# Optimization experiments

Hardware: AMD Instinct MI355X
Metric: run time of the kernel (lower is better)

The kernel has to match this reference:

```python
import jax, jax.numpy as jnp
import numpy as np

NEG_SLOPE = 0.01  # torch F.leaky_relu_ default


def setup_inputs() -> dict:
    key = jax.random.key(0)
    k1, k2, k3, k4, k5 = jax.random.split(key, 5)
    N, Fin, Fout = 8192, 256, 128
    X = jax.random.normal(k1, (N, Fin), dtype=jnp.float32)
    adj = jax.random.randint(k2, (N, N), 0, 2, dtype=jnp.int32)
    W = jax.random.normal(k3, (Fout, Fin), dtype=jnp.float32) * 0.05
    b = jax.random.normal(k4, (Fout,), dtype=jnp.float32) * 0.05
    S = jax.random.normal(k5, (2 * Fout,), dtype=jnp.float32)
    return {"X": X, "adj": adj, "W": W, "b": b, "S": S}


def reference(X, adj, W, b, S):
    # X' = W X + b  -> (N, Fout)
    Xp = X @ W.T + b
    N, Fout = Xp.shape
    S_src, S_dst = S[:Fout], S[Fout:]
    # e_ij = leaky_relu(S . [x'_i ; x'_j]) = leaky_relu(S_src.x'_i + S_dst.x'_j)
    e = jax.nn.leaky_relu(
        (Xp @ S_src)[:, None] + (Xp @ S_dst)[None, :], NEG_SLOPE
    )  # (N, N)
    # neighbor set = nonzero entries of adj row plus self-loop
    mask = (adj != 0) | jnp.eye(N, dtype=bool)
    e = jnp.where(mask, e, -jnp.inf)
    attn = jax.nn.softmax(e, axis=1)  # segment softmax over each row's neighbors
    out = jax.nn.sigmoid(attn @ Xp)  # (N, Fout)
    return out
```

## Files before the change

kernel.cpp:

```cpp
#include <hip/hip_runtime.h>

typedef unsigned short u16;
typedef __attribute__((ext_vector_type(8))) u16 u16x8;
typedef __attribute__((ext_vector_type(8))) __bf16 bf16x8;
typedef __attribute__((ext_vector_type(4))) float f32x4;

#define NN 8192
#define FIN 256
#define FOUT 128

__device__ __forceinline__ u16 f2bf(float f) {
  unsigned u = __float_as_uint(f);
  u += 0x7fffu + ((u >> 16) & 1u);
  return (u16)(u >> 16);
}
__device__ __forceinline__ float bf2f(u16 s) {
  return __uint_as_float(((unsigned)s) << 16);
}

__global__ __launch_bounds__(256) void k_splitw(const float* __restrict__ W,
                                                u16* __restrict__ Whi,
                                                u16* __restrict__ Wlo) {
  int t = blockIdx.x * 256 + threadIdx.x;
  float w = W[t];
  u16 hi = f2bf(w);
  Whi[t] = hi;
  Wlo[t] = f2bf(w - bf2f(hi));
}

__global__ __launch_bounds__(256) void k_xp(const float* __restrict__ X,
    const u16* __restrict__ Whi, const u16* __restrict__ Wlo,
    const float* __restrict__ bias, const float* __restrict__ S,
    u16* __restrict__ Bsw, float* __restrict__ alphaA, float* __restrict__ cexpA,
    float* __restrict__ jbF, u16* __restrict__ jebA, u16* __restrict__ jeb2A) {
  __shared__ float Xs[32 * 129];
  __shared__ float Ss[256];
  const int tid = threadIdx.x;
  Ss[tid] = S[tid];
  const int i0 = blockIdx.x * 32;
  const int w = tid >> 6, l = tid & 63;
  const int mt = w & 1, nh = w >> 1;
  const int li = l & 15, quad = l >> 4;
  const int row = i0 + mt * 16 + li;

  f32x4 acc[4];
#pragma unroll
  for (int nt4 = 0; nt4 < 4; ++nt4) acc[nt4] = f32x4{0.f, 0.f, 0.f, 0.f};

  const float* xrow = X + (size_t)row * FIN + quad * 8;
  for (int k0 = 0; k0 < FIN; k0 += 32) {
    float4 xa = *(const float4*)(xrow + k0);
    float4 xb = *(const float4*)(xrow + k0 + 4);
    float xv[8] = {xa.x, xa.y, xa.z, xa.w, xb.x, xb.y, xb.z, xb.w};
    u16x8 ahiu, alou;
#pragma unroll
    for (int jj = 0; jj < 8; ++jj) {
      u16 h = f2bf(xv[jj]);
      ahiu[jj] = h;
      alou[jj] = f2bf(xv[jj] - bf2f(h));
    }
    bf16x8 ahi = __builtin_bit_cast(bf16x8, ahiu);
    bf16x8 alo = __builtin_bit_cast(bf16x8, alou);
#pragma unroll
    for (int nt4 = 0; nt4 < 4; ++nt4) {
      int f = nh * 64 + nt4 * 16 + li;
      size_t wofs = (size_t)f * FIN + k0 + quad * 8;
      bf16x8 bhi = __builtin_bit_cast(bf16x8, *(const u16x8*)(Whi + wofs));
      bf16x8 blo = __builtin_bit_cast(bf16x8, *(const u16x8*)(Wlo + wofs));
      acc[nt4] = __builtin_amdgcn_mfma_f32_16x16x32_bf16(ahi, bhi, acc[nt4], 0, 0, 0);
      acc[nt4] = __builtin_amdgcn_mfma_f32_16x16x32_bf16(alo, bhi, acc[nt4], 0, 0, 0);
      acc[nt4] = __builtin_amdgcn_mfma_f32_16x16x32_bf16(ahi, blo, acc[nt4], 0, 0, 0);
    }
  }
#pragma unroll
  for (int nt4 = 0; nt4 < 4; ++nt4) {
    int f = nh * 64 + nt4 * 16 + li;
    float bv = bias[f];
#pragma unroll
    for (int r = 0; r < 4; ++r)
      Xs[(mt * 16 + quad * 4 + r) * 129 + f] = acc[nt4][r] + bv;
  }
  __syncthreads();

#pragma unroll
  for (int s = 0; s < 2; ++s) {
    int nt = w + s * 4;
    int f = nt * 16 + li;
    int jl = quad * 8;
    u16x8 ou;
#pragma unroll
    for (int jj = 0; jj < 8; ++jj) ou[jj] = f2bf(Xs[(jl + jj) * 129 + f]);
    *(u16x8*)(Bsw + (((size_t)(i0 >> 5)) * 8 + nt) * 512 + (size_t)l * 8) = ou;
  }

  const int r = tid >> 3, sub = tid & 7;
  float pa = 0.f, pb = 0.f;
#pragma unroll
  for (int m = 0; m < 16; ++m) {
    int f = sub + m * 8;
    float x = Xs[r * 129 + f];
    pa += x * Ss[f];
    pb += x * Ss[128 + f];
  }
  pa += __shfl_xor(pa, 1); pa += __shfl_xor(pa, 2); pa += __shfl_xor(pa, 4);
  pb += __shfl_xor(pb, 1); pb += __shfl_xor(pb, 2); pb += __shfl_xor(pb, 4);
  if (sub == 0) {
    int i = i0 + r;
    alphaA[i] = pa;
    cexpA[i] = expf(-0.99f * pa);
    jbF[i] = pb;
    jebA[i] = f2bf(expf(pb));
    jeb2A[i] = f2bf(expf(0.01f * pb));
  }
}

__global__ __launch_bounds__(512, 2) void k_gat(const int* __restrict__ adj,
    const u16* __restrict__ Bsw, const float* __restrict__ alphaA,
    const float* __restrict__ cexpA, const float* __restrict__ jbF,
    const u16* __restrict__ jebA, const u16* __restrict__ jeb2A,
    float* __restrict__ out) {
  __shared__ float sacc[32 * 132];
  __shared__ float sden[32];
  const int tid = threadIdx.x;
  for (int t = tid; t < 32 * 132; t += 512) sacc[t] = 0.f;
  if (tid < 32) sden[tid] = 0.f;
  __syncthreads();

  const int w = tid >> 6, l = tid & 63;
  const int li = l & 15, quad = l >> 4;
  const int i0 = blockIdx.x * 32;
  const int im0 = i0 + li, im1 = im0 + 16;
  const float nega0 = -alphaA[im0], nega1 = -alphaA[im1];
  const float c0 = cexpA[im0], c1 = cexpA[im1];
  const int* ar0 = adj + (size_t)im0 * NN;
  const int* ar1 = adj + (size_t)im1 * NN;

  f32x4 acc0[8], acc1[8];
#pragma unroll
  for (int nt = 0; nt < 8; ++nt) {
    acc0[nt] = f32x4{0.f, 0.f, 0.f, 0.f};
    acc1[nt] = f32x4{0.f, 0.f, 0.f, 0.f};
  }
  float den0 = 0.f, den1 = 0.f;

  const int jbeg = w * 1024, jend = jbeg + 1024;
  for (int j0 = jbeg; j0 < jend; j0 += 32) {
    const int jq = j0 + quad * 8;
    int4 a00 = *(const int4*)(ar0 + jq);
    int4 a01 = *(const int4*)(ar0 + jq + 4);
    int4 a10 = *(const int4*)(ar1 + jq);
    int4 a11 = *(const int4*)(ar1 + jq + 4);
    float4 b0 = *(const float4*)(jbF + jq);
    float4 b1 = *(const float4*)(jbF + jq + 4);
    u16x8 ebj = *(const u16x8*)(jebA + jq);
    u16x8 e2j = *(const u16x8*)(jeb2A + jq);
    int a0v[8] = {a00.x, a00.y, a00.z, a00.w, a01.x, a01.y, a01.z, a01.w};
    int a1v[8] = {a10.x, a10.y, a10.z, a10.w, a11.x, a11.y, a11.z, a11.w};
    float bv[8] = {b0.x, b0.y, b0.z, b0.w, b1.x, b1.y, b1.z, b1.w};
    u16x8 af0, af1;
#pragma unroll
    for (int jj = 0; jj < 8; ++jj) {
      float bf = bv[jj];
      float eb = bf2f(ebj[jj]);
      float e2 = bf2f(e2j[jj]);
      int jg = jq + jj;
      float w0 = (bf >= nega0) ? eb : c0 * e2;
      w0 = (a0v[jj] != 0 || jg == im0) ? w0 : 0.f;
      u16 q0 = f2bf(w0);
      af0[jj] = q0;
      den0 += bf2f(q0);
      float w1 = (bf >= nega1) ? eb : c1 * e2;
      w1 = (a1v[jj] != 0 || jg == im1) ? w1 : 0.f;
      u16 q1 = f2bf(w1);
      af1[jj] = q1;
      den1 += bf2f(q1);
    }
    bf16x8 A0 = __builtin_bit_cast(bf16x8, af0);
    bf16x8 A1 = __builtin_bit_cast(bf16x8, af1);
    const u16* bb = Bsw + ((size_t)(j0 >> 5) * 8) * 512 + (size_t)l * 8;
#pragma unroll
    for (int nt = 0; nt < 8; ++nt) {
      bf16x8 B = __builtin_bit_cast(bf16x8, *(const u16x8*)(bb + nt * 512));
      acc0[nt] = __builtin_amdgcn_mfma_f32_16x16x32_bf16(A0, B, acc0[nt], 0, 0, 0);
      acc1[nt] = __builtin_amdgcn_mfma_f32_16x16x32_bf16(A1, B, acc1[nt], 0, 0, 0);
    }
  }

  den0 += __shfl_xor(den0, 16); den0 += __shfl_xor(den0, 32);
  den1 += __shfl_xor(den1, 16); den1 += __shfl_xor(den1, 32);
  if (l < 16) { atomicAdd(&sden[li], den0); atomicAdd(&sden[16 + li], den1); }

#pragma unroll
  for (int nt = 0; nt < 8; ++nt) {
#pragma unroll
    for (int r = 0; r < 4; ++r) {
      atomicAdd(&sacc[(quad * 4 + r) * 132 + nt * 16 + li], acc0[nt][r]);
      atomicAdd(&sacc[(16 + quad * 4 + r) * 132 + nt * 16 + li], acc1[nt][r]);
    }
  }
  __syncthreads();

  const int orow = l & 31, fh = l >> 5;
  const int fbase = w * 16 + fh * 8;
  const float* p = &sacc[orow * 132 + fbase];
  float4 v0 = *(const float4*)p;
  float4 v1 = *(const float4*)(p + 4);
  float rd = 1.f / sden[orow];
  float o[8] = {v0.x, v0.y, v0.z, v0.w, v1.x, v1.y, v1.z, v1.w};
#pragma unroll
  for (int jj = 0; jj < 8; ++jj) {
    float v = o[jj] * rd;
    o[jj] = 1.f / (1.f + __expf(-v));
  }
  float* op = out + (size_t)(i0 + orow) * FOUT + fbase;
  *(float4*)op = make_float4(o[0], o[1], o[2], o[3]);
  *(float4*)(op + 4) = make_float4(o[4], o[5], o[6], o[7]);
}

extern "C" void kernel_launch(void* const* d_in, const int* in_sizes, int n_in,
                              void* d_out, int out_size, void* d_ws, size_t ws_size,
                              hipStream_t stream) {
  const float* X = (const float*)d_in[0];
  const int* adj = (const int*)d_in[1];
  const float* W = (const float*)d_in[2];
  const float* bias = (const float*)d_in[3];
  const float* S = (const float*)d_in[4];
  float* out = (float*)d_out;

  char* ws = (char*)d_ws;
  u16* Bsw     = (u16*)(ws);
  u16* Whi     = (u16*)(ws + 2097152);
  u16* Wlo     = (u16*)(ws + 2162688);
  float* alphaA = (float*)(ws + 2228224);
  float* cexpA  = (float*)(ws + 2260992);
  float* jbF    = (float*)(ws + 2293760);
  u16* jebA    = (u16*)(ws + 2326528);
  u16* jeb2A   = (u16*)(ws + 2342912);

  hipLaunchKernelGGL(k_splitw, dim3(128), dim3(256), 0, stream, W, Whi, Wlo);
  hipLaunchKernelGGL(k_xp, dim3(256), dim3(256), 0, stream, X, Whi, Wlo, bias, S,
                     Bsw, alphaA, cexpA, jbF, jebA, jeb2A);
  hipLaunchKernelGGL(k_gat, dim3(256), dim3(512), 0, stream, adj, Bsw, alphaA, cexpA,
                     jbF, jebA, jeb2A, out);
}
```

Before: 476.0 us.

## Restructure GAT kernels: max-based weights, MFMA denominator, diagonal precompute, prefetch

The attention weight uses max(exp(b_j), c_i*exp(0.01 b_j)), which equals the leaky-relu exponential, so the per-element comparison and the alpha/jb arrays are no longer needed. The self-loop is handled by a precomputed diagonal weight that seeds the accumulators, so the per-element index comparison goes away. The row-sum denominator is computed with an extra MFMA against a ones vector instead of scalar adds. Both kernels now use 16 rows per block with twice as many blocks, adj loads are software-prefetched one iteration ahead, and truncation replaces rounding for the bf16 pack. This trades the reuse of B tiles across two row groups for more parallelism and a lighter inner loop, with small numeric differences from the truncation.

```diff
diff --git a/kernel.cpp b/kernel.cpp
--- a/kernel.cpp
+++ b/kernel.cpp
@@ -13,6 +13,9 @@
   unsigned u = __float_as_uint(f);
   u += 0x7fffu + ((u >> 16) & 1u);
   return (u16)(u >> 16);
+}
+__device__ __forceinline__ u16 f2bft(float f) {
+  return (u16)(__float_as_uint(f) >> 16);
 }
 __device__ __forceinline__ float bf2f(u16 s) {
   return __uint_as_float(((unsigned)s) << 16);
@@ -31,26 +34,32 @@
 __global__ __launch_bounds__(256) void k_xp(const float* __restrict__ X,
     const u16* __restrict__ Whi, const u16* __restrict__ Wlo,
     const float* __restrict__ bias, const float* __restrict__ S,
-    u16* __restrict__ Bsw, float* __restrict__ alphaA, float* __restrict__ cexpA,
-    float* __restrict__ jbF, u16* __restrict__ jebA, u16* __restrict__ jeb2A) {
-  __shared__ float Xs[32 * 129];
+    const int* __restrict__ adj,
+    u16* __restrict__ Bsw, float* __restrict__ cexpA,
+    u16* __restrict__ jebA, u16* __restrict__ jeb2A, float* __restrict__ diagW) {
+  __shared__ float Xs[16 * 260];
+  __shared__ float Xp[16 * 132];
   __shared__ float Ss[256];
   const int tid = threadIdx.x;
+  const int i0 = blockIdx.x * 16;
   Ss[tid] = S[tid];
-  const int i0 = blockIdx.x * 32;
-  const int w = tid >> 6, l = tid & 63;
-  const int mt = w & 1, nh = w >> 1;
-  const int li = l & 15, quad = l >> 4;
-  const int row = i0 + mt * 16 + li;
-
-  f32x4 acc[4];
-#pragma unroll
-  for (int nt4 = 0; nt4 < 4; ++nt4) acc[nt4] = f32x4{0.f, 0.f, 0.f, 0.f};
-
-  const float* xrow = X + (size_t)row * FIN + quad * 8;
+  {
+    int r = tid >> 4, c = (tid & 15) * 16;
+    const float* src = X + (size_t)(i0 + r) * FIN + c;
+    float* dst = Xs + r * 260 + c;
+#pragma unroll
+    for (int k = 0; k < 16; k += 4) *(float4*)(dst + k) = *(const float4*)(src + k);
+  }
+  __syncthreads();
+
+  const int w = tid >> 6, l = tid & 63, li = l & 15, quad = l >> 4;
+  f32x4 acc[2];
+  acc[0] = f32x4{0.f, 0.f, 0.f, 0.f};
+  acc[1] = f32x4{0.f, 0.f, 0.f, 0.f};
   for (int k0 = 0; k0 < FIN; k0 += 32) {
-    float4 xa = *(const float4*)(xrow + k0);
-    float4 xb = *(const float4*)(xrow + k0 + 4);
+    const float* xp = Xs + li * 260 + k0 + quad * 8;
+    float4 xa = *(const float4*)xp;
+    float4 xb = *(const float4*)(xp + 4);
     float xv[8] = {xa.x, xa.y, xa.z, xa.w, xb.x, xb.y, xb.z, xb.w};
     u16x8 ahiu, alou;
 #pragma unroll
@@ -62,159 +71,179 @@
     bf16x8 ahi = __builtin_bit_cast(bf16x8, ahiu);
     bf16x8 alo = __builtin_bit_cast(bf16x8, alou);
 #pragma unroll
-    for (int nt4 = 0; nt4 < 4; ++nt4) {
-      int f = nh * 64 + nt4 * 16 + li;
+    for (int t2 = 0; t2 < 2; ++t2) {
+      int f = (w * 2 + t2) * 16 + li;
       size_t wofs = (size_t)f * FIN + k0 + quad * 8;
       bf16x8 bhi = __builtin_bit_cast(bf16x8, *(const u16x8*)(Whi + wofs));
       bf16x8 blo = __builtin_bit_cast(bf16x8, *(const u16x8*)(Wlo + wofs));
-      acc[nt4] = __builtin_amdgcn_mfma_f32_16x16x32_bf16(ahi, bhi, acc[nt4], 0, 0, 0);
-      acc[nt4] = __builtin_amdgcn_mfma_f32_16x16x32_bf16(alo, bhi, acc[nt4], 0, 0, 0);
-      acc[nt4] = __builtin_amdgcn_mfma_f32_16x16x32_bf16(ahi, blo, acc[nt4], 0, 0, 0);
-    }
-  }
-#pragma unroll
-  for (int nt4 = 0; nt4 < 4; ++nt4) {
-    int f = nh * 64 + nt4 * 16 + li;
+      acc[t2] = __builtin_amdgcn_mfma_f32_16x16x32_bf16(ahi, bhi, acc[t2], 0, 0, 0);
+      acc[t2] = __builtin_amdgcn_mfma_f32_16x16x32_bf16(alo, bhi, acc[t2], 0, 0, 0);
+      acc[t2] = __builtin_amdgcn_mfma_f32_16x16x32_bf16(ahi, blo, acc[t2], 0, 0, 0);
+    }
+  }
+#pragma unroll
+  for (int t2 = 0; t2 < 2; ++t2) {
+    int f = (w * 2 + t2) * 16 + li;
     float bv = bias[f];
 #pragma unroll
     for (int r = 0; r < 4; ++r)
-      Xs[(mt * 16 + quad * 4 + r) * 129 + f] = acc[nt4][r] + bv;
-  }
-  __syncthreads();
-
-#pragma unroll
-  for (int s = 0; s < 2; ++s) {
-    int nt = w + s * 4;
-    int f = nt * 16 + li;
-    int jl = quad * 8;
+      Xp[(quad * 4 + r) * 132 + f] = acc[t2][r] + bv;
+  }
+  __syncthreads();
+
+  {
+    int li2 = tid & 15, q2sub = (tid >> 4) & 1, nt = tid >> 5;
+    int f = nt * 16 + li2;
+    int rb = q2sub * 8;
+    int q2 = ((i0 & 16) >> 3) + q2sub;
     u16x8 ou;
 #pragma unroll
-    for (int jj = 0; jj < 8; ++jj) ou[jj] = f2bf(Xs[(jl + jj) * 129 + f]);
-    *(u16x8*)(Bsw + (((size_t)(i0 >> 5)) * 8 + nt) * 512 + (size_t)l * 8) = ou;
-  }
-
-  const int r = tid >> 3, sub = tid & 7;
-  float pa = 0.f, pb = 0.f;
-#pragma unroll
-  for (int m = 0; m < 16; ++m) {
-    int f = sub + m * 8;
-    float x = Xs[r * 129 + f];
-    pa += x * Ss[f];
-    pb += x * Ss[128 + f];
-  }
-  pa += __shfl_xor(pa, 1); pa += __shfl_xor(pa, 2); pa += __shfl_xor(pa, 4);
-  pb += __shfl_xor(pb, 1); pb += __shfl_xor(pb, 2); pb += __shfl_xor(pb, 4);
-  if (sub == 0) {
+    for (int jj = 0; jj < 8; ++jj) ou[jj] = f2bf(Xp[(rb + jj) * 132 + f]);
+    *(u16x8*)(Bsw + ((size_t)(i0 >> 5) * 8 + nt) * 512 + (size_t)(q2 * 16 + li2) * 8) = ou;
+  }
+
+  {
+    int r = tid >> 4, sub = tid & 15;
+    float pa = 0.f, pb = 0.f;
+#pragma unroll
+    for (int m = 0; m < 8; ++m) {
+      float x = Xp[r * 132 + sub + m * 16];
+      pa += x * Ss[sub + m * 16];
+      pb += x * Ss[128 + sub + m * 16];
+    }
+    pa += __shfl_xor(pa, 1); pa += __shfl_xor(pa, 2);
+    pa += __shfl_xor(pa, 4); pa += __shfl_xor(pa, 8);
+    pb += __shfl_xor(pb, 1); pb += __shfl_xor(pb, 2);
+    pb += __shfl_xor(pb, 4); pb += __shfl_xor(pb, 8);
+    if (sub == 0) {
+      int i = i0 + r;
+      float cc = expf(-0.99f * pa);
+      u16 ebq = f2bf(expf(pb));
+      u16 e2q = f2bf(expf(0.01f * pb));
+      cexpA[i] = cc;
+      jebA[i] = ebq;
+      jeb2A[i] = e2q;
+      float wii = fmaxf(bf2f(ebq), cc * bf2f(e2q));
+      float wq = bf2f(f2bft(wii));
+      int ad = adj[(size_t)i * NN + i];
+      diagW[i] = (ad != 0) ? 0.f : wq;
+    }
+  }
+}
+
+__global__ __launch_bounds__(512, 4) void k_gat(const int* __restrict__ adj,
+    const u16* __restrict__ Bsw, const float* __restrict__ cexpA,
+    const u16* __restrict__ jebA, const u16* __restrict__ jeb2A,
+    const float* __restrict__ diagW, float* __restrict__ out) {
+  __shared__ float sacc[16 * 132];
+  __shared__ float sden[16];
+  const int tid = threadIdx.x;
+  const int i0 = blockIdx.x * 16;
+
+  {
+    int r = tid >> 5, f = (tid & 31) * 4;
     int i = i0 + r;
-    alphaA[i] = pa;
-    cexpA[i] = expf(-0.99f * pa);
-    jbF[i] = pb;
-    jebA[i] = f2bf(expf(pb));
-    jeb2A[i] = f2bf(expf(0.01f * pb));
-  }
-}
-
-__global__ __launch_bounds__(512, 2) void k_gat(const int* __restrict__ adj,
-    const u16* __restrict__ Bsw, const float* __restrict__ alphaA,
-    const float* __restrict__ cexpA, const float* __restrict__ jbF,
-    const u16* __restrict__ jebA, const u16* __restrict__ jeb2A,
-    float* __restrict__ out) {
-  __shared__ float sacc[32 * 132];
-  __shared__ float sden[32];
-  const int tid = threadIdx.x;
-  for (int t = tid; t < 32 * 132; t += 512) sacc[t] = 0.f;
-  if (tid < 32) sden[tid] = 0.f;
-  __syncthreads();
-
-  const int w = tid >> 6, l = tid & 63;
-  const int li = l & 15, quad = l >> 4;
-  const int i0 = blockIdx.x * 32;
-  const int im0 = i0 + li, im1 = im0 + 16;
-  const float nega0 = -alphaA[im0], nega1 = -alphaA[im1];
-  const float c0 = cexpA[im0], c1 = cexpA[im1];
-  const int* ar0 = adj + (size_t)im0 * NN;
-  const int* ar1 = adj + (size_t)im1 * NN;
-
-  f32x4 acc0[8], acc1[8];
-#pragma unroll
-  for (int nt = 0; nt < 8; ++nt) {
-    acc0[nt] = f32x4{0.f, 0.f, 0.f, 0.f};
-    acc1[nt] = f32x4{0.f, 0.f, 0.f, 0.f};
-  }
-  float den0 = 0.f, den1 = 0.f;
+    float dw = diagW[i];
+    size_t slotbase = (size_t)(i0 >> 5) * 8;
+    int laneq = ((i & 31) >> 3) * 16;
+    int elem = i & 7;
+    float4 v;
+    float* vp = &v.x;
+#pragma unroll
+    for (int k = 0; k < 4; ++k) {
+      int ff = f + k;
+      u16 xb = Bsw[(slotbase + (ff >> 4)) * 512 + (size_t)(laneq + (ff & 15)) * 8 + elem];
+      vp[k] = dw * bf2f(xb);
+    }
+    *(float4*)&sacc[r * 132 + f] = v;
+    if (tid < 16) sden[tid] = diagW[i0 + tid];
+  }
+  __syncthreads();
+
+  const int w = tid >> 6, l = tid & 63, li = l & 15, quad = l >> 4;
+  const int im = i0 + li;
+  const float c = cexpA[im];
+  const int* ar = adj + (size_t)im * NN;
+
+  f32x4 acc[8];
+#pragma unroll
+  for (int nt = 0; nt < 8; ++nt) acc[nt] = f32x4{0.f, 0.f, 0.f, 0.f};
+  f32x4 accD = f32x4{0.f, 0.f, 0.f, 0.f};
+
+  u16x8 onesu;
+#pragma unroll
+  for (int jj = 0; jj < 8; ++jj) onesu[jj] = 0x3F80;
+  const bf16x8 ONES = __builtin_bit_cast(bf16x8, onesu);
 
   const int jbeg = w * 1024, jend = jbeg + 1024;
+  const int qofs = quad * 8;
+
+  int4 ca0, ca1;
+  u16x8 ceb, ce2;
+  {
+    const int jq = jbeg + qofs;
+    ca0 = *(const int4*)(ar + jq);
+    ca1 = *(const int4*)(ar + jq + 4);
+    ceb = *(const u16x8*)(jebA + jq);
+    ce2 = *(const u16x8*)(jeb2A + jq);
+  }
   for (int j0 = jbeg; j0 < jend; j0 += 32) {
-    const int jq = j0 + quad * 8;
-    int4 a00 = *(const int4*)(ar0 + jq);
-    int4 a01 = *(const int4*)(ar0 + jq + 4);
-    int4 a10 = *(const int4*)(ar1 + jq);
-    int4 a11 = *(const int4*)(ar1 + jq + 4);
-    float4 b0 = *(const float4*)(jbF + jq);
-    float4 b1 = *(const float4*)(jbF + jq + 4);
-    u16x8 ebj = *(const u16x8*)(jebA + jq);
-    u16x8 e2j = *(const u16x8*)(jeb2A + jq);
-    int a0v[8] = {a00.x, a00.y, a00.z, a00.w, a01.x, a01.y, a01.z, a01.w};
-    int a1v[8] = {a10.x, a10.y, a10.z, a10.w, a11.x, a11.y, a11.z, a11.w};
-    float bv[8] = {b0.x, b0.y, b0.z, b0.w, b1.x, b1.y, b1.z, b1.w};
-    u16x8 af0, af1;
+    const int jn = (j0 + 32 < jend) ? (j0 + 32) : jbeg;
+    const int jq = jn + qofs;
+    int4 na0 = *(const int4*)(ar + jq);
+    int4 na1 = *(const int4*)(ar + jq + 4);
+    u16x8 neb = *(const u16x8*)(jebA + jq);
+    u16x8 ne2 = *(const u16x8*)(jeb2A + jq);
+
+    int av[8] = {ca0.x, ca0.y, ca0.z, ca0.w, ca1.x, ca1.y, ca1.z, ca1.w};
+    float wv[8];
 #pragma unroll
     for (int jj = 0; jj < 8; ++jj) {
-      float bf = bv[jj];
-      float eb = bf2f(ebj[jj]);
-      float e2 = bf2f(e2j[jj]);
-      int jg = jq + jj;
-      float w0 = (bf >= nega0) ? eb : c0 * e2;
-      w0 = (a0v[jj] != 0 || jg == im0) ? w0 : 0.f;
-      u16 q0 = f2bf(w0);
-      af0[jj] = q0;
-      den0 += bf2f(q0);
-      float w1 = (bf >= nega1) ? eb : c1 * e2;
-      w1 = (a1v[jj] != 0 || jg == im1) ? w1 : 0.f;
-      u16 q1 = f2bf(w1);
-      af1[jj] = q1;
-      den1 += bf2f(q1);
-    }
-    bf16x8 A0 = __builtin_bit_cast(bf16x8, af0);
-    bf16x8 A1 = __builtin_bit_cast(bf16x8, af1);
-    const u16* bb = Bsw + ((size_t)(j0 >> 5) * 8) * 512 + (size_t)l * 8;
+      float ww = fmaxf(bf2f(ceb[jj]), c * bf2f(ce2[jj]));
+      wv[jj] = (av[jj] != 0) ? ww : 0.f;
+    }
+    unsigned pk[4];
+#pragma unroll
+    for (int p = 0; p < 4; ++p)
+      pk[p] = __builtin_amdgcn_perm(__float_as_uint(wv[2 * p + 1]),
+                                    __float_as_uint(wv[2 * p]), 0x07060302u);
+    bf16x8 A = __builtin_bit_cast(bf16x8, *(u16x8*)pk);
+
+    const u16* bb = Bsw + (size_t)(j0 >> 5) * 4096 + (size_t)l * 8;
 #pragma unroll
     for (int nt = 0; nt < 8; ++nt) {
       bf16x8 B = __builtin_bit_cast(bf16x8, *(const u16x8*)(bb + nt * 512));
-      acc0[nt] = __builtin_amdgcn_mfma_f32_16x16x32_bf16(A0, B, acc0[nt], 0, 0, 0);
-      acc1[nt] = __builtin_amdgcn_mfma_f32_16x16x32_bf16(A1, B, acc1[nt], 0, 0, 0);
-    }
-  }
-
-  den0 += __shfl_xor(den0, 16); den0 += __shfl_xor(den0, 32);
-  den1 += __shfl_xor(den1, 16); den1 += __shfl_xor(den1, 32);
-  if (l < 16) { atomicAdd(&sden[li], den0); atomicAdd(&sden[16 + li], den1); }
-
+      acc[nt] = __builtin_amdgcn_mfma_f32_16x16x32_bf16(A, B, acc[nt], 0, 0, 0);
+    }
+    accD = __builtin_amdgcn_mfma_f32_16x16x32_bf16(A, ONES, accD, 0, 0, 0);
+
+    ca0 = na0; ca1 = na1; ceb = neb; ce2 = ne2;
+  }
+
+  if (li == 0) {
+#pragma unroll
+    for (int r = 0; r < 4; ++r) atomicAdd(&sden[quad * 4 + r], accD[r]);
+  }
 #pragma unroll
   for (int nt = 0; nt < 8; ++nt) {
 #pragma unroll
-    for (int r = 0; r < 4; ++r) {
-      atomicAdd(&sacc[(quad * 4 + r) * 132 + nt * 16 + li], acc0[nt][r]);
-      atomicAdd(&sacc[(16 + quad * 4 + r) * 132 + nt * 16 + li], acc1[nt][r]);
-    }
-  }
-  __syncthreads();
-
-  const int orow = l & 31, fh = l >> 5;
-  const int fbase = w * 16 + fh * 8;
-  const float* p = &sacc[orow * 132 + fbase];
-  float4 v0 = *(const float4*)p;
-  float4 v1 = *(const float4*)(p + 4);
-  float rd = 1.f / sden[orow];
-  float o[8] = {v0.x, v0.y, v0.z, v0.w, v1.x, v1.y, v1.z, v1.w};
-#pragma unroll
-  for (int jj = 0; jj < 8; ++jj) {
-    float v = o[jj] * rd;
-    o[jj] = 1.f / (1.f + __expf(-v));
-  }
-  float* op = out + (size_t)(i0 + orow) * FOUT + fbase;
-  *(float4*)op = make_float4(o[0], o[1], o[2], o[3]);
-  *(float4*)(op + 4) = make_float4(o[4], o[5], o[6], o[7]);
+    for (int r = 0; r < 4; ++r)
+      atomicAdd(&sacc[(quad * 4 + r) * 132 + nt * 16 + li], acc[nt][r]);
+  }
+  __syncthreads();
+
+  {
+    int r = tid >> 5, c4 = (tid & 31) * 4;
+    float4 v = *(const float4*)&sacc[r * 132 + c4];
+    float rd = 1.f / sden[r];
+    float o[4] = {v.x, v.y, v.z, v.w};
+#pragma unroll
+    for (int k = 0; k < 4; ++k) {
+      float t = o[k] * rd;
+      o[k] = 1.f / (1.f + __expf(-t));
+    }
+    *(float4*)(out + (size_t)(i0 + r) * FOUT + c4) = make_float4(o[0], o[1], o[2], o[3]);
+  }
 }
 
 extern "C" void kernel_launch(void* const* d_in, const int* in_sizes, int n_in,
@@ -228,18 +257,17 @@
   float* out = (float*)d_out;
 
   char* ws = (char*)d_ws;
-  u16* Bsw     = (u16*)(ws);
-  u16* Whi     = (u16*)(ws + 2097152);
-  u16* Wlo     = (u16*)(ws + 2162688);
-  float* alphaA = (float*)(ws + 2228224);
-  float* cexpA  = (float*)(ws + 2260992);
-  float* jbF    = (float*)(ws + 2293760);
-  u16* jebA    = (u16*)(ws + 2326528);
-  u16* jeb2A   = (u16*)(ws + 2342912);
+  u16* Bsw      = (u16*)(ws);
+  u16* Whi      = (u16*)(ws + 2097152);
+  u16* Wlo      = (u16*)(ws + 2162688);
+  float* cexpA  = (float*)(ws + 2228224);
+  u16* jebA     = (u16*)(ws + 2260992);
+  u16* jeb2A    = (u16*)(ws + 2277376);
+  float* diagW  = (float*)(ws + 2293760);
 
   hipLaunchKernelGGL(k_splitw, dim3(128), dim3(256), 0, stream, W, Whi, Wlo);
-  hipLaunchKernelGGL(k_xp, dim3(256), dim3(256), 0, stream, X, Whi, Wlo, bias, S,
-                     Bsw, alphaA, cexpA, jbF, jebA, jeb2A);
-  hipLaunchKernelGGL(k_gat, dim3(256), dim3(512), 0, stream, adj, Bsw, alphaA, cexpA,
-                     jbF, jebA, jeb2A, out);
-}
+  hipLaunchKernelGGL(k_xp, dim3(512), dim3(256), 0, stream, X, Whi, Wlo, bias, S, adj,
+                     Bsw, cexpA, jebA, jeb2A, diagW);
+  hipLaunchKernelGGL(k_gat, dim3(512), dim3(512), 0, stream, adj, Bsw, cexpA,
+                     jebA, jeb2A, diagW, out);
+}
```

Result: no change. 476.8 us (+0.2%).
